# Kernel optimization log

Hardware: AMD Instinct MI355X
Metric: run time of the kernel (lower is better)

Reference implementation:

```python
import jax, jax.numpy as jnp
import numpy as np

OUT, IN, GS = 16384, 4096, 16
G = OUT * IN // GS  # 4194304 groups


def setup_inputs() -> dict:
    key = jax.random.key(0)
    k1, k2, k3, k4 = jax.random.split(key, 4)
    x = jax.random.normal(k1, (8, 32, IN), dtype=jnp.float32)
    weight_q2 = jax.random.randint(k2, (G, GS // 4), 0, 256, dtype=jnp.int32)
    weight_norm = jax.random.uniform(k3, (G, 1), dtype=jnp.float16)
    bias = jax.random.normal(k4, (OUT,), dtype=jnp.float32)
    return {"x": x, "weight_q2": weight_q2, "weight_norm": weight_norm, "bias": bias}


def _dequant_2bit(weight_q2, weight_norm):
    # torch: xq_out[:, i::4] = (xq >> 2i) & 3  =>  element index within group = i + 4*k
    # where k = packed column (slow, stride 4), i = shift index (fast).
    norm = weight_norm.astype(jnp.float32)                      # [G, 1]
    shifts = jnp.arange(4, dtype=jnp.int32) * 2                 # [4]
    vals = (weight_q2[:, :, None] >> shifts) & 3                # [G, 4(pack k), 4(shift i)]
    xq_out = vals.astype(jnp.float32).reshape(G, GS)            # [G, 16], layout k*4 + i
    w = (xq_out / 3.0) * (2.0 * norm) - norm                    # [G, 16]
    return w.reshape(OUT, IN)


def reference(x, weight_q2, weight_norm, bias):
    w = _dequant_2bit(weight_q2, weight_norm)                   # [OUT, IN] fp32
    return jnp.einsum('bsi,oi->bso', x, w) + bias
```

## Files before the change

kernel.cpp:

```cpp
#include <hip/hip_runtime.h>
#include <stdint.h>

#define M_DIM 256
#define N_DIM 16384
#define K_DIM 4096
#define BN 64
#define BK 64
#define NT (K_DIM / BK)

typedef __bf16 bf16x8 __attribute__((ext_vector_type(8)));
typedef float  f32x4  __attribute__((ext_vector_type(4)));

__device__ __forceinline__ uint32_t f2bf(float f) {
  uint32_t u = __float_as_uint(f);
  return (u + 0x7fffu + ((u >> 16) & 1u)) >> 16;
}

__global__ __launch_bounds__(256) void cvt_x_kernel(const float* __restrict__ x,
                                                    uint4* __restrict__ ws) {
  int T = blockIdx.x * 256 + threadIdx.x;
  int mb_glob = T >> 13;
  int r       = T & 8191;
  int kch     = r >> 6;
  int L       = r & 63;
  int row = mb_glob * 16 + (L & 15);
  int k   = kch * 32 + (L >> 4) * 8;
  const float* p = x + (size_t)row * K_DIM + k;
  float4 a = *(const float4*)p;
  float4 b = *(const float4*)(p + 4);
  uint4 o;
  o.x = f2bf(a.x) | (f2bf(a.y) << 16);
  o.y = f2bf(a.z) | (f2bf(a.w) << 16);
  o.z = f2bf(b.x) | (f2bf(b.y) << 16);
  o.w = f2bf(b.z) | (f2bf(b.w) << 16);
  ws[T] = o;
}

__device__ __forceinline__ uint4 deq8(uint2 q, float nv) {
  float a2 = nv * (2.0f / 3.0f);
  uint32_t tlo = f2bf(-nv) | (f2bf(fmaf(1.0f, a2, -nv)) << 16);
  uint32_t thi = f2bf(fmaf(2.0f, a2, -nv)) | (f2bf(fmaf(3.0f, a2, -nv)) << 16);
  uint32_t s0 = ((q.x & 3u) | ((q.x & 0xCu) << 14)) * 0x0202u + 0x01000100u;
  uint32_t s1 = (((q.x >> 4) & 3u) | ((q.x & 0xC0u) << 10)) * 0x0202u + 0x01000100u;
  uint32_t s2 = ((q.y & 3u) | ((q.y & 0xCu) << 14)) * 0x0202u + 0x01000100u;
  uint32_t s3 = (((q.y >> 4) & 3u) | ((q.y & 0xC0u) << 10)) * 0x0202u + 0x01000100u;
  uint4 r;
  r.x = __builtin_amdgcn_perm(thi, tlo, s0);
  r.y = __builtin_amdgcn_perm(thi, tlo, s1);
  r.z = __builtin_amdgcn_perm(thi, tlo, s2);
  r.w = __builtin_amdgcn_perm(thi, tlo, s3);
  return r;
}

__global__ __launch_bounds__(512, 2) void gemm2bit_kernel(
    const uint4*    __restrict__ aws,
    const uint32_t* __restrict__ q2,
    const float*    __restrict__ nrm,
    const float*    __restrict__ bias,
    float*          __restrict__ out)
{
  __shared__ uint4 Bb[2][512];
  __shared__ uint4 Sc[2048];

  const int tid  = threadIdx.x;
  const int lane = tid & 63;
  const int w    = tid >> 6;
  const int wm   = w >> 1;
  const int tw   = w & 1;
  const int lo4  = lane & 15;
  const int qd   = lane >> 4;
  const int n0   = blockIdx.x * BN;

  const int nloc = tid >> 3;
  const int kg   = (tid >> 1) & 3;
  const int h    = tid & 1;
  const int grow = n0 + nloc;
  const int bslot = ((kg >> 1) * 4 + (nloc >> 4)) * 64 + (kg & 1) * 32 + h * 16 + (nloc & 15);

  const uint4* pA = aws + (((size_t)(wm * 4) * 128 + tw) * 64 + lane);
  const uint32_t* pq = q2 + ((size_t)grow * 256 + kg) * 4 + h * 2;
  const float*    pn = nrm + (size_t)grow * 256 + kg;

  f32x4 acc[4][4];
#pragma unroll
  for (int s = 0; s < 4; ++s)
#pragma unroll
    for (int u = 0; u < 4; ++u)
      acc[s][u] = (f32x4){0.f, 0.f, 0.f, 0.f};

  uint4 af0[4], af1[4];
  uint2 qA, qB;
  float nA, nB;

#pragma unroll
  for (int s = 0; s < 4; ++s) af0[s] = pA[(size_t)s * 8192];
  uint2 q0 = *(const uint2*)pq;
  float n0v = pn[0];
  qA = *(const uint2*)(pq + 16);
  nA = pn[4];
  Bb[0][bslot] = deq8(q0, n0v);
  __syncthreads();

#define GEMM_BODY(T, PR, AFC, AFN, QC, NC, QN, NN)                              \
  do {                                                                          \
    if ((T) + 1 < NT) {                                                         \
      size_t toff = (size_t)((T) + 1) * 128;                                    \
      _Pragma("unroll")                                                         \
      for (int s = 0; s < 4; ++s) AFN[s] = pA[(size_t)s * 8192 + toff];         \
    }                                                                           \
    if ((T) + 2 < NT) {                                                         \
      QN = *(const uint2*)(pq + (size_t)((T) + 2) * 16);                        \
      NN = pn[(size_t)((T) + 2) * 4];                                           \
    }                                                                           \
    bf16x8 bfv[4];                                                              \
    _Pragma("unroll")                                                           \
    for (int u = 0; u < 4; ++u)                                                 \
      bfv[u] = *(const bf16x8*)&Bb[PR][(tw * 4 + u) * 64 + lane];               \
    _Pragma("unroll")                                                           \
    for (int s = 0; s < 4; ++s) {                                               \
      bf16x8 av = __builtin_bit_cast(bf16x8, AFC[s]);                           \
      _Pragma("unroll")                                                         \
      for (int u = 0; u < 4; ++u)                                               \
        acc[s][u] = __builtin_amdgcn_mfma_f32_16x16x32_bf16(av, bfv[u],         \
                                                            acc[s][u], 0, 0, 0);\
    }                                                                           \
    if ((T) + 1 < NT) Bb[(PR) ^ 1][bslot] = deq8(QC, NC);                       \
    __syncthreads();                                                            \
  } while (0)

  for (int t2 = 0; t2 < NT; t2 += 2) {
    GEMM_BODY(t2,     0, af0, af1, qA, nA, qB, nB);
    GEMM_BODY(t2 + 1, 1, af1, af0, qB, nB, qA, nA);
  }
#undef GEMM_BODY

  float bv[4];
#pragma unroll
  for (int u = 0; u < 4; ++u) bv[u] = bias[n0 + u * 16 + lo4];

  if (tw == 1) {
#pragma unroll
    for (int s = 0; s < 2; ++s)
#pragma unroll
      for (int u = 0; u < 4; ++u)
        Sc[((wm * 2 + s) * 4 + u) * 64 + lane] = __builtin_bit_cast(uint4, acc[s][u]);
  }
  __syncthreads();
  if (tw == 0) {
#pragma unroll
    for (int s = 0; s < 2; ++s)
#pragma unroll
      for (int u = 0; u < 4; ++u) {
        f32x4 o = acc[s][u] +
                  __builtin_bit_cast(f32x4, Sc[((wm * 2 + s) * 4 + u) * 64 + lane]);
        int mrow = wm * 64 + s * 16 + qd * 4;
        float* p = out + (size_t)mrow * N_DIM + (n0 + u * 16 + lo4);
#pragma unroll
        for (int r = 0; r < 4; ++r) p[(size_t)r * N_DIM] = o[r] + bv[u];
      }
  }
  __syncthreads();
  if (tw == 0) {
#pragma unroll
    for (int s = 2; s < 4; ++s)
#pragma unroll
      for (int u = 0; u < 4; ++u)
        Sc[((wm * 2 + (s - 2)) * 4 + u) * 64 + lane] = __builtin_bit_cast(uint4, acc[s][u]);
  }
  __syncthreads();
  if (tw == 1) {
#pragma unroll
    for (int s = 2; s < 4; ++s)
#pragma unroll
      for (int u = 0; u < 4; ++u) {
        f32x4 o = acc[s][u] +
                  __builtin_bit_cast(f32x4, Sc[((wm * 2 + (s - 2)) * 4 + u) * 64 + lane]);
        int mrow = wm * 64 + s * 16 + qd * 4;
        float* p = out + (size_t)mrow * N_DIM + (n0 + u * 16 + lo4);
#pragma unroll
        for (int r = 0; r < 4; ++r) p[(size_t)r * N_DIM] = o[r] + bv[u];
      }
  }
}

extern "C" void kernel_launch(void* const* d_in, const int* in_sizes, int n_in,
                              void* d_out, int out_size, void* d_ws, size_t ws_size,
                              hipStream_t stream) {
  const float*    x    = (const float*)d_in[0];
  const uint32_t* q2   = (const uint32_t*)d_in[1];
  const float*    nm   = (const float*)d_in[2];
  const float*    bias = (const float*)d_in[3];
  float*          out  = (float*)d_out;
  uint4*          aws  = (uint4*)d_ws;

  cvt_x_kernel<<<512, 256, 0, stream>>>(x, aws);
  gemm2bit_kernel<<<dim3(N_DIM / BN, 1), 512, 0, stream>>>(aws, q2, nm, bias, out);
}
```

Measured before the change: 166.9 us.

## Split M across two blocks and drop split-K warp reduction

The GEMM grid now has two blocks along M, each covering 128 rows. Each warp owns a 32x32 output tile with full K, so the shared-memory split-K reduction and its extra barriers go away. The launch bound is raised to four blocks per CU to match the smaller accumulator footprint, and the B tile in LDS is XOR-swizzled to cut bank conflicts. In exchange, the 2-bit weights are dequantized twice, once per M-half, which doubles weight loads and dequant work.

```diff
diff --git a/kernel.cpp b/kernel.cpp
--- a/kernel.cpp
+++ b/kernel.cpp
@@ -52,7 +52,7 @@
   return r;
 }
 
-__global__ __launch_bounds__(512, 2) void gemm2bit_kernel(
+__global__ __launch_bounds__(512, 4) void gemm2bit_kernel(
     const uint4*    __restrict__ aws,
     const uint32_t* __restrict__ q2,
     const float*    __restrict__ nrm,
@@ -60,32 +60,36 @@
     float*          __restrict__ out)
 {
   __shared__ uint4 Bb[2][512];
-  __shared__ uint4 Sc[2048];
 
   const int tid  = threadIdx.x;
   const int lane = tid & 63;
   const int w    = tid >> 6;
   const int wm   = w >> 1;
-  const int tw   = w & 1;
+  const int wn   = w & 1;
   const int lo4  = lane & 15;
   const int qd   = lane >> 4;
   const int n0   = blockIdx.x * BN;
+  const int m0   = blockIdx.y * 128;
+
+  const int lrs = lane ^ qd;
 
   const int nloc = tid >> 3;
   const int kg   = (tid >> 1) & 3;
   const int h    = tid & 1;
   const int grow = n0 + nloc;
-  const int bslot = ((kg >> 1) * 4 + (nloc >> 4)) * 64 + (kg & 1) * 32 + h * 16 + (nloc & 15);
+  const int qd2   = (kg & 1) * 2 + h;
+  const int bslot = ((kg >> 1) * 4 + (nloc >> 4)) * 64 + qd2 * 16 +
+                    ((nloc & 15) ^ qd2);
 
-  const uint4* pA = aws + (((size_t)(wm * 4) * 128 + tw) * 64 + lane);
+  const uint4* pA = aws + ((size_t)(blockIdx.y * 8 + wm * 2) * 128) * 64 + lane;
   const uint32_t* pq = q2 + ((size_t)grow * 256 + kg) * 4 + h * 2;
   const float*    pn = nrm + (size_t)grow * 256 + kg;
 
-  f32x4 acc[4][4];
+  f32x4 acc[2][2];
 #pragma unroll
-  for (int s = 0; s < 4; ++s)
+  for (int s = 0; s < 2; ++s)
 #pragma unroll
-    for (int u = 0; u < 4; ++u)
+    for (int u = 0; u < 2; ++u)
       acc[s][u] = (f32x4){0.f, 0.f, 0.f, 0.f};
 
   uint4 af0[4], af1[4];
@@ -93,7 +97,10 @@
   float nA, nB;
 
 #pragma unroll
-  for (int s = 0; s < 4; ++s) af0[s] = pA[(size_t)s * 8192];
+  for (int s = 0; s < 2; ++s)
+#pragma unroll
+    for (int ts = 0; ts < 2; ++ts)
+      af0[s * 2 + ts] = pA[(size_t)s * 8192 + ts * 64];
   uint2 q0 = *(const uint2*)pq;
   float n0v = pn[0];
   qA = *(const uint2*)(pq + 16);
@@ -106,23 +113,29 @@
     if ((T) + 1 < NT) {                                                         \
       size_t toff = (size_t)((T) + 1) * 128;                                    \
       _Pragma("unroll")                                                         \
-      for (int s = 0; s < 4; ++s) AFN[s] = pA[(size_t)s * 8192 + toff];         \
+      for (int s = 0; s < 2; ++s)                                               \
+        _Pragma("unroll")                                                       \
+        for (int ts = 0; ts < 2; ++ts)                                          \
+          AFN[s * 2 + ts] = pA[(size_t)s * 8192 + toff + ts * 64];              \
     }                                                                           \
     if ((T) + 2 < NT) {                                                         \
       QN = *(const uint2*)(pq + (size_t)((T) + 2) * 16);                        \
       NN = pn[(size_t)((T) + 2) * 4];                                           \
     }                                                                           \
-    bf16x8 bfv[4];                                                              \
     _Pragma("unroll")                                                           \
-    for (int u = 0; u < 4; ++u)                                                 \
-      bfv[u] = *(const bf16x8*)&Bb[PR][(tw * 4 + u) * 64 + lane];               \
-    _Pragma("unroll")                                                           \
-    for (int s = 0; s < 4; ++s) {                                               \
-      bf16x8 av = __builtin_bit_cast(bf16x8, AFC[s]);                           \
+    for (int ts = 0; ts < 2; ++ts) {                                            \
+      bf16x8 bfv[2];                                                            \
       _Pragma("unroll")                                                         \
-      for (int u = 0; u < 4; ++u)                                               \
-        acc[s][u] = __builtin_amdgcn_mfma_f32_16x16x32_bf16(av, bfv[u],         \
-                                                            acc[s][u], 0, 0, 0);\
+      for (int u = 0; u < 2; ++u)                                               \
+        bfv[u] = *(const bf16x8*)&Bb[PR][(ts * 4 + wn * 2 + u) * 64 + lrs];     \
+      _Pragma("unroll")                                                         \
+      for (int s = 0; s < 2; ++s) {                                             \
+        bf16x8 av = __builtin_bit_cast(bf16x8, AFC[s * 2 + ts]);                \
+        _Pragma("unroll")                                                       \
+        for (int u = 0; u < 2; ++u)                                             \
+          acc[s][u] = __builtin_amdgcn_mfma_f32_16x16x32_bf16(av, bfv[u],       \
+                                                              acc[s][u], 0, 0, 0);\
+      }                                                                         \
     }                                                                           \
     if ((T) + 1 < NT) Bb[(PR) ^ 1][bslot] = deq8(QC, NC);                       \
     __syncthreads();                                                            \
@@ -134,52 +147,22 @@
   }
 #undef GEMM_BODY
 
-  float bv[4];
+  float bv[2];
 #pragma unroll
-  for (int u = 0; u < 4; ++u) bv[u] = bias[n0 + u * 16 + lo4];
+  for (int u = 0; u < 2; ++u)
+    bv[u] = bias[n0 + wn * 32 + u * 16 + lo4];
 
-  if (tw == 1) {
 #pragma unroll
-    for (int s = 0; s < 2; ++s)
+  for (int s = 0; s < 2; ++s) {
+    int mrow = m0 + wm * 32 + s * 16 + qd * 4;
 #pragma unroll
-      for (int u = 0; u < 4; ++u)
-        Sc[((wm * 2 + s) * 4 + u) * 64 + lane] = __builtin_bit_cast(uint4, acc[s][u]);
-  }
-  __syncthreads();
-  if (tw == 0) {
+    for (int u = 0; u < 2; ++u) {
+      int ncol = n0 + wn * 32 + u * 16 + lo4;
+      float* p = out + (size_t)mrow * N_DIM + ncol;
 #pragma unroll
-    for (int s = 0; s < 2; ++s)
-#pragma unroll
-      for (int u = 0; u < 4; ++u) {
-        f32x4 o = acc[s][u] +
-                  __builtin_bit_cast(f32x4, Sc[((wm * 2 + s) * 4 + u) * 64 + lane]);
-        int mrow = wm * 64 + s * 16 + qd * 4;
-        float* p = out + (size_t)mrow * N_DIM + (n0 + u * 16 + lo4);
-#pragma unroll
-        for (int r = 0; r < 4; ++r) p[(size_t)r * N_DIM] = o[r] + bv[u];
-      }
-  }
-  __syncthreads();
-  if (tw == 0) {
-#pragma unroll
-    for (int s = 2; s < 4; ++s)
-#pragma unroll
-      for (int u = 0; u < 4; ++u)
-        Sc[((wm * 2 + (s - 2)) * 4 + u) * 64 + lane] = __builtin_bit_cast(uint4, acc[s][u]);
-  }
-  __syncthreads();
-  if (tw == 1) {
-#pragma unroll
-    for (int s = 2; s < 4; ++s)
-#pragma unroll
-      for (int u = 0; u < 4; ++u) {
-        f32x4 o = acc[s][u] +
-                  __builtin_bit_cast(f32x4, Sc[((wm * 2 + (s - 2)) * 4 + u) * 64 + lane]);
-        int mrow = wm * 64 + s * 16 + qd * 4;
-        float* p = out + (size_t)mrow * N_DIM + (n0 + u * 16 + lo4);
-#pragma unroll
-        for (int r = 0; r < 4; ++r) p[(size_t)r * N_DIM] = o[r] + bv[u];
-      }
+      for (int r = 0; r < 4; ++r)
+        p[(size_t)r * N_DIM] = acc[s][u][r] + bv[u];
+    }
   }
 }
 
@@ -194,5 +177,5 @@
   uint4*          aws  = (uint4*)d_ws;
 
   cvt_x_kernel<<<512, 256, 0, stream>>>(x, aws);
-  gemm2bit_kernel<<<dim3(N_DIM / BN, 1), 512, 0, stream>>>(aws, q2, nm, bias, out);
+  gemm2bit_kernel<<<dim3(N_DIM / BN, 2), 512, 0, stream>>>(aws, q2, nm, bias, out);
 }
```

Result: no change. 164.0 us (-1.7%).
